# Optimization experiments

Hardware: AMD Instinct MI355X
Metric: run time of the kernel (lower is better)

## Reference

```python
import jax, jax.numpy as jnp
import numpy as np

N_NODES = 60000
N_EDGES = 240000
N_REL = 4
N_GRAPHS = 128
D_IN = 768
D_H = 256
N_LAYERS = 6


def setup_inputs() -> dict:
    key = jax.random.key(0)
    ks = jax.random.split(key, 16)
    x = jax.random.normal(ks[0], (N_NODES, D_IN), dtype=jnp.float32)
    edge_index = jax.random.randint(ks[1], (2, N_EDGES), 0, N_NODES, dtype=jnp.int64)
    edge_attr = jax.random.randint(ks[2], (N_EDGES,), 0, N_REL, dtype=jnp.int64)
    batch = jnp.sort(jax.random.randint(ks[3], (N_NODES,), 0, N_GRAPHS, dtype=jnp.int64))
    s0 = 1.0 / np.sqrt(D_IN)
    s1 = 1.0 / np.sqrt(D_H)
    w0 = jax.random.normal(ks[4], (N_REL, D_IN, D_H), dtype=jnp.float32) * s0
    root0 = jax.random.normal(ks[5], (D_IN, D_H), dtype=jnp.float32) * s0
    b0 = jnp.zeros((D_H,), jnp.float32)
    w_rest = jax.random.normal(ks[6], (N_LAYERS - 1, N_REL, D_H, D_H), dtype=jnp.float32) * s1
    root_rest = jax.random.normal(ks[7], (N_LAYERS - 1, D_H, D_H), dtype=jnp.float32) * s1
    b_rest = jnp.zeros((N_LAYERS - 1, D_H), jnp.float32)
    fc1_w = jax.random.normal(ks[8], (2 * D_H, 128), dtype=jnp.float32) * (1.0 / np.sqrt(2 * D_H))
    fc1_b = jnp.zeros((128,), jnp.float32)
    fc2_w = jax.random.normal(ks[9], (128, 1), dtype=jnp.float32) * (1.0 / np.sqrt(128))
    fc2_b = jnp.zeros((1,), jnp.float32)
    return {"x": x, "edge_index": edge_index, "edge_attr": edge_attr, "batch": batch,
            "w0": w0, "root0": root0, "b0": b0,
            "w_rest": w_rest, "root_rest": root_rest, "b_rest": b_rest,
            "fc1_w": fc1_w, "fc1_b": fc1_b, "fc2_w": fc2_w, "fc2_b": fc2_b}


def _rgcn(h, src, dst, rel, W, root, b):
    # PyG RGCNConv with aggr='mean': per-relation mean over incoming edges,
    # transformed by per-relation weight, plus root transform and bias.
    n = h.shape[0]
    seg = rel * n + dst                                   # combined (relation, target) segment id
    msgs = h[src]                                         # [E, d_in] gather
    agg = jax.ops.segment_sum(msgs, seg, num_segments=N_REL * n)
    agg = agg.reshape(N_REL, n, -1)                       # [R, N, d_in]
    cnt = jax.ops.segment_sum(jnp.ones_like(rel, jnp.float32), seg, num_segments=N_REL * n)
    cnt = cnt.reshape(N_REL, n, 1)
    mean = agg / jnp.maximum(cnt, 1.0)                    # mean aggregation; 0 for isolated nodes
    return jnp.einsum('rnd,rdo->no', mean, W) + h @ root + b


def reference(x, edge_index, edge_attr, batch, w0, root0, b0,
              w_rest, root_rest, b_rest, fc1_w, fc1_b, fc2_w, fc2_b):
    src, dst = edge_index[0], edge_index[1]
    h = jax.nn.relu(_rgcn(x, src, dst, edge_attr, w0, root0, b0))
    for i in range(N_LAYERS - 1):
        h = jax.nn.relu(_rgcn(h, src, dst, edge_attr, w_rest[i], root_rest[i], b_rest[i]))
    # global mean / max pooling over graphs
    sums = jax.ops.segment_sum(h, batch, num_segments=N_GRAPHS)
    cnt = jax.ops.segment_sum(jnp.ones((h.shape[0],), jnp.float32), batch, num_segments=N_GRAPHS)[:, None]
    h_mean = sums / jnp.maximum(cnt, 1.0)
    h_max = jax.ops.segment_max(h, batch, num_segments=N_GRAPHS)
    h_max = jnp.where(cnt > 0, h_max, 0.0)
    g = jnp.concatenate([h_mean, h_max], axis=1)          # [G, 512]
    out = jax.nn.relu(g @ fc1_w + fc1_b)                  # dropout is identity at inference
    out = out @ fc2_w + fc2_b
    return jax.nn.sigmoid(out.squeeze(-1))                # [G]
```

## Files before the change

kernel.cpp:

```cpp
#include <hip/hip_runtime.h>
#include <hip/hip_bf16.h>

#define N_NODES  60000
#define N_EDGES  240000
#define N_REL    4
#define N_GRAPHS 128
#define D_IN     768
#define D_H      256
#define N_LAYERS 6
#define M_PAD    60032
#define N_TOT    1280
#define BM_L     64
#define LDM      264

static inline int cdiv(int a, int b) { return (a + b - 1) / b; }

typedef __attribute__((ext_vector_type(8))) short short8;
typedef __attribute__((ext_vector_type(4))) float f32x4;

__device__ __forceinline__ float bf2f(unsigned short u) {
    union { unsigned int i; float f; } c; c.i = ((unsigned int)u) << 16; return c.f;
}
__device__ __forceinline__ float bflo(unsigned int u) {
    union { unsigned int i; float f; } c; c.i = u << 16; return c.f;
}
__device__ __forceinline__ float bfhi(unsigned int u) {
    union { unsigned int i; float f; } c; c.i = u & 0xffff0000u; return c.f;
}
__device__ __forceinline__ unsigned short f2bf(float f) {
    union { float f; unsigned int i; } c; c.f = f;
    unsigned int i = c.i;
    unsigned int r = (i + 0x7FFFu + ((i >> 16) & 1u)) >> 16;
    return (unsigned short)r;
}

__device__ __forceinline__ void gload16(const void* g, void* l) {
    __builtin_amdgcn_global_load_lds((const __attribute__((address_space(1))) void*)g,
                                     (__attribute__((address_space(3))) void*)l, 16, 0, 0);
}

__device__ __forceinline__ void accum32(float4* am, uint4 v0, uint4 v1, uint4 v2, uint4 v3) {
    am[0].x += bflo(v0.x); am[0].y += bfhi(v0.x);
    am[0].z += bflo(v0.y); am[0].w += bfhi(v0.y);
    am[1].x += bflo(v0.z); am[1].y += bfhi(v0.z);
    am[1].z += bflo(v0.w); am[1].w += bfhi(v0.w);
    am[2].x += bflo(v1.x); am[2].y += bfhi(v1.x);
    am[2].z += bflo(v1.y); am[2].w += bfhi(v1.y);
    am[3].x += bflo(v1.z); am[3].y += bfhi(v1.z);
    am[3].z += bflo(v1.w); am[3].w += bfhi(v1.w);
    am[4].x += bflo(v2.x); am[4].y += bfhi(v2.x);
    am[4].z += bflo(v2.y); am[4].w += bfhi(v2.y);
    am[5].x += bflo(v2.z); am[5].y += bfhi(v2.z);
    am[5].z += bflo(v2.w); am[5].w += bfhi(v2.w);
    am[6].x += bflo(v3.x); am[6].y += bfhi(v3.x);
    am[6].z += bflo(v3.y); am[6].w += bfhi(v3.y);
    am[7].x += bflo(v3.z); am[7].y += bfhi(v3.z);
    am[7].z += bflo(v3.w); am[7].w += bfhi(v3.w);
}

__global__ __launch_bounds__(512) void gemm_l0(
    const unsigned short* __restrict__ A,
    const unsigned short* __restrict__ Bt,
    const float* __restrict__ bias,
    unsigned short* __restrict__ out_root,
    unsigned short* __restrict__ out_msg,
    int K)
{
    __shared__ unsigned short As[128 * 32];
    __shared__ unsigned short Bs[256 * 32];

    const int tid  = threadIdx.x;
    const int wave = tid >> 6, lane = tid & 63;

    int b = blockIdx.x;
    int bm, bn;
    if (b < 2320) { int grp = b / 40, rem = b % 40; bm = (grp * 8 + (rem & 7)) * 128; bn = (rem >> 3) * 256; }
    else          { int rem = b - 2320; bm = (464 + rem % 5) * 128; bn = (rem / 5) * 256; }

    const int wm = (wave & 1) * 64, wn = (wave >> 1) * 64;

    const int lr = lane >> 2;
    const int kg = ((lane & 3) ^ ((lr ^ (lr >> 2)) & 3)) * 8;
    const unsigned short* gsrc[3];
    unsigned short* ldst[3];
    #pragma unroll
    for (int j = 0; j < 3; ++j) {
        int g = wave * 3 + j;
        if (g < 8) {
            gsrc[j] = A + (size_t)(bm + g * 16 + lr) * K + kg;
            ldst[j] = As + g * 16 * 32;
        } else {
            gsrc[j] = Bt + (size_t)(bn + (g - 8) * 16 + lr) * K + kg;
            ldst[j] = Bs + (g - 8) * 16 * 32;
        }
    }

    f32x4 acc[4][4] = {};
    const int fr = lane & 15;
    const int qsw = (((lane >> 4) ^ fr ^ (fr >> 2)) & 3) * 8;

    for (int k0 = 0; k0 < K; k0 += 32) {
        gload16(gsrc[0] + k0, ldst[0]);
        gload16(gsrc[1] + k0, ldst[1]);
        gload16(gsrc[2] + k0, ldst[2]);
        __syncthreads();

        short8 a[4], bb[4];
        #pragma unroll
        for (int t = 0; t < 4; ++t) {
            a[t]  = *(const short8*)&As[(wm + t * 16 + fr) * 32 + qsw];
            bb[t] = *(const short8*)&Bs[(wn + t * 16 + fr) * 32 + qsw];
        }
        #pragma unroll
        for (int mt = 0; mt < 4; ++mt)
            #pragma unroll
            for (int nt = 0; nt < 4; ++nt)
                acc[mt][nt] = __builtin_amdgcn_mfma_f32_16x16x32_bf16(
                    a[mt], bb[nt], acc[mt][nt], 0, 0, 0);
        __syncthreads();
    }

    const bool is_root = (bn == 0);
    #pragma unroll
    for (int mt = 0; mt < 4; ++mt) {
        #pragma unroll
        for (int nt = 0; nt < 4; ++nt) {
            int col = bn + wn + nt * 16 + fr;
            float bv = bias[col];
            #pragma unroll
            for (int r = 0; r < 4; ++r) {
                int row = bm + wm + mt * 16 + ((lane >> 4) << 2) + r;
                float v = acc[mt][nt][r] + bv;
                if (is_root) out_root[(size_t)row * 256 + col] = f2bf(v);
                else         out_msg[(size_t)row * 1024 + (col - 256)] = f2bf(v);
            }
        }
    }
}

__global__ __launch_bounds__(512) void rgcn_layer(
    const unsigned short* __restrict__ h,
    const unsigned short* __restrict__ Wl,
    const float* __restrict__ bias,
    const int* __restrict__ rp4,
    const int* __restrict__ e_srcs,
    const float* __restrict__ inv4,
    unsigned short* __restrict__ h_out)
{
    __shared__ unsigned short mt[BM_L * LDM];
    __shared__ unsigned short Bs[256 * 32];

    const int tid  = threadIdx.x;
    const int wave = tid >> 6, lane = tid & 63;
    const int bm = blockIdx.x * BM_L;

    const int node  = bm + lane;
    const int cq    = wave * 32;
    const bool valid = node < N_NODES;

    const int lr = lane >> 2;
    const int kg = ((lane & 3) ^ ((lr ^ (lr >> 2)) & 3)) * 8;

    const int fr  = lane & 15;
    const int q8  = (lane >> 4) * 8;
    const int qsw = (((lane >> 4) ^ fr ^ (fr >> 2)) & 3) * 8;
    const int wcol = wave * 32;

    float4 iv = valid ? *(const float4*)&inv4[(size_t)node * 4]
                      : make_float4(1.f, 1.f, 1.f, 1.f);

    f32x4 acc[4][2] = {};

    for (int r = 0; r < 5; ++r) {
        float4 am[8];
        #pragma unroll
        for (int j = 0; j < 8; ++j) am[j] = make_float4(0.f, 0.f, 0.f, 0.f);

        if (r < 4) {
            if (valid) {
                int lo = rp4[(size_t)node * 4 + r];
                int hi = rp4[(size_t)node * 4 + r + 1];
                int e = lo;
                for (; e + 1 < hi; e += 2) {
                    const uint4* p0 = (const uint4*)(h + (size_t)e_srcs[e] * 256 + cq);
                    const uint4* p1 = (const uint4*)(h + (size_t)e_srcs[e + 1] * 256 + cq);
                    uint4 v0 = p0[0], v1 = p0[1], v2 = p0[2], v3 = p0[3];
                    uint4 u0 = p1[0], u1 = p1[1], u2 = p1[2], u3 = p1[3];
                    accum32(am, v0, v1, v2, v3);
                    accum32(am, u0, u1, u2, u3);
                }
                if (e < hi) {
                    const uint4* p0 = (const uint4*)(h + (size_t)e_srcs[e] * 256 + cq);
                    accum32(am, p0[0], p0[1], p0[2], p0[3]);
                }
            }
        } else {
            const uint4* p0 = (const uint4*)(h + (size_t)node * 256 + cq);
            accum32(am, p0[0], p0[1], p0[2], p0[3]);
        }
        float sc = (r == 0) ? iv.x : (r == 1) ? iv.y : (r == 2) ? iv.z
                 : (r == 3) ? iv.w : 1.f;

        __syncthreads();
        {
            unsigned short* dst = &mt[lane * LDM + cq];
            #pragma unroll
            for (int j = 0; j < 8; ++j) {
                ushort4 o;
                o.x = f2bf(am[j].x * sc); o.y = f2bf(am[j].y * sc);
                o.z = f2bf(am[j].z * sc); o.w = f2bf(am[j].w * sc);
                *(ushort4*)(dst + j * 4) = o;
            }
        }

        const int rOff = r << 8;
        #pragma unroll 1
        for (int kk = 0; kk < 8; ++kk) {
            if (kk > 0) __syncthreads();
            {
                int g0 = wave * 2;
                gload16(Wl + (size_t)(g0 * 16 + lr) * N_TOT + rOff + kg + kk * 32,
                        Bs + g0 * 512);
                gload16(Wl + (size_t)((g0 + 1) * 16 + lr) * N_TOT + rOff + kg + kk * 32,
                        Bs + (g0 + 1) * 512);
            }
            __syncthreads();

            short8 a4[4], b0, b1;
            #pragma unroll
            for (int i = 0; i < 4; ++i)
                a4[i] = *(const short8*)&mt[(i * 16 + fr) * LDM + kk * 32 + q8];
            b0 = *(const short8*)&Bs[(wcol + fr) * 32 + qsw];
            b1 = *(const short8*)&Bs[(wcol + 16 + fr) * 32 + qsw];
            #pragma unroll
            for (int i = 0; i < 4; ++i) {
                acc[i][0] = __builtin_amdgcn_mfma_f32_16x16x32_bf16(a4[i], b0, acc[i][0], 0, 0, 0);
                acc[i][1] = __builtin_amdgcn_mfma_f32_16x16x32_bf16(a4[i], b1, acc[i][1], 0, 0, 0);
            }
        }
        __syncthreads();
    }

    #pragma unroll
    for (int i = 0; i < 4; ++i) {
        #pragma unroll
        for (int nt = 0; nt < 2; ++nt) {
            int col = wcol + nt * 16 + fr;
            float bv = bias[col];
            #pragma unroll
            for (int rg = 0; rg < 4; ++rg) {
                int row = bm + i * 16 + ((lane >> 4) << 2) + rg;
                float v = fmaxf(acc[i][nt][rg] + bv, 0.f);
                h_out[(size_t)row * 256 + col] = f2bf(v);
            }
        }
    }
}

__global__ void convert_x(const float* __restrict__ x, unsigned short* __restrict__ xb) {
    size_t i = ((size_t)blockIdx.x * 256 + threadIdx.x) * 4;
    if (i >= (size_t)M_PAD * D_IN) return;
    ushort4 o;
    if (i < (size_t)N_NODES * D_IN) {
        float4 v = *(const float4*)&x[i];
        o.x = f2bf(v.x); o.y = f2bf(v.y); o.z = f2bf(v.z); o.w = f2bf(v.w);
    } else {
        o.x = o.y = o.z = o.w = 0;
    }
    *(ushort4*)&xb[i] = o;
}

__global__ __launch_bounds__(256) void pack_w0_t(
    const float* __restrict__ root0, const float* __restrict__ w0,
    unsigned short* __restrict__ Wt0)
{
    __shared__ float t[32][33];
    int b = blockIdx.x;
    int i  = b / 192;
    int rem = b % 192;
    int kb = (rem / 8) * 32;
    int nb = (rem % 8) * 32;
    const float* S = (i == 0) ? root0 : w0 + (size_t)(i - 1) * D_IN * 256;
    int tx = threadIdx.x & 31, ty = threadIdx.x >> 5;
    #pragma unroll
    for (int j = 0; j < 4; ++j)
        t[ty + j * 8][tx] = S[(size_t)(kb + ty + j * 8) * 256 + nb + tx];
    __syncthreads();
    #pragma unroll
    for (int j = 0; j < 4; ++j)
        Wt0[(size_t)(i * 256 + nb + ty + j * 8) * D_IN + kb + tx] = f2bf(t[tx][ty + j * 8]);
}

__global__ __launch_bounds__(256) void pack_wr_t(
    const float* __restrict__ root_rest, const float* __restrict__ w_rest,
    unsigned short* __restrict__ WtR)
{
    __shared__ float t[32][33];
    int b = blockIdx.x;
    int m = b / 64;
    int rem = b % 64;
    int kb = (rem / 8) * 32;
    int nb = (rem % 8) * 32;
    int l = m / 5, j = m % 5;
    const float* S = (j < 4) ? w_rest + (size_t)(l * 4 + j) * 256 * 256
                             : root_rest + (size_t)l * 256 * 256;
    int tx = threadIdx.x & 31, ty = threadIdx.x >> 5;
    #pragma unroll
    for (int jj = 0; jj < 4; ++jj)
        t[ty + jj * 8][tx] = S[(size_t)(kb + ty + jj * 8) * 256 + nb + tx];
    __syncthreads();
    #pragma unroll
    for (int jj = 0; jj < 4; ++jj)
        WtR[(size_t)(l * 256 + nb + ty + jj * 8) * N_TOT + j * 256 + kb + tx] =
            f2bf(t[tx][ty + jj * 8]);
}

__global__ void build_bias(const float* __restrict__ b0, float* __restrict__ eb) {
    int i = blockIdx.x * 256 + threadIdx.x;
    if (i < N_TOT) eb[i] = (i < 256) ? b0[i] : 0.f;
}

__global__ void deg4_count(const int* __restrict__ dst, const int* __restrict__ rel,
                           int* __restrict__ deg4, int E) {
    int e = blockIdx.x * 256 + threadIdx.x;
    if (e < E) atomicAdd(&deg4[dst[e] * 4 + rel[e]], 1);
}

__global__ void invert4(const int* __restrict__ deg4, float* __restrict__ inv4, int n) {
    int i = blockIdx.x * 256 + threadIdx.x;
    if (i < n) inv4[i] = 1.0f / (float)max(deg4[i], 1);
}

__global__ __launch_bounds__(256) void block_sum(const int* __restrict__ deg,
                                                 int* __restrict__ bsum, int n) {
    __shared__ int s[256];
    int i = blockIdx.x * 256 + threadIdx.x;
    s[threadIdx.x] = (i < n) ? deg[i] : 0;
    __syncthreads();
    for (int o = 128; o > 0; o >>= 1) {
        if (threadIdx.x < o) s[threadIdx.x] += s[threadIdx.x + o];
        __syncthreads();
    }
    if (threadIdx.x == 0) bsum[blockIdx.x] = s[0];
}

__global__ __launch_bounds__(1024) void scan_bsum(const int* __restrict__ bsum,
                                                  int* __restrict__ boff, int nb) {
    __shared__ int s[1024];
    int t = threadIdx.x;
    int v0 = (t < nb) ? bsum[t] : 0;
    s[t] = v0;
    __syncthreads();
    for (int o = 1; o < 1024; o <<= 1) {
        int v = (t >= o) ? s[t - o] : 0;
        __syncthreads();
        s[t] += v;
        __syncthreads();
    }
    if (t < nb) boff[t] = s[t] - v0;
}

__global__ __launch_bounds__(256) void block_scan_write(
    const int* __restrict__ deg, const int* __restrict__ boff,
    int* __restrict__ row_ptr, int* __restrict__ cursor, int n, int total) {
    __shared__ int s[256];
    int t = threadIdx.x;
    int i = blockIdx.x * 256 + t;
    int v = (i < n) ? deg[i] : 0;
    s[t] = v;
    __syncthreads();
    for (int o = 1; o < 256; o <<= 1) {
        int u = (t >= o) ? s[t - o] : 0;
        __syncthreads();
        s[t] += u;
        __syncthreads();
    }
    int excl = s[t] - v + boff[blockIdx.x];
    if (i < n) { row_ptr[i] = excl; cursor[i] = excl; }
    if (blockIdx.x == 0 && t == 0) row_ptr[n] = total;
}

__global__ void place_edges4(const int* __restrict__ dst, const int* __restrict__ src,
                             const int* __restrict__ rel, int* __restrict__ cursor,
                             int* __restrict__ e_srcs, int E) {
    int e = blockIdx.x * 256 + threadIdx.x;
    if (e < E) {
        int p = atomicAdd(&cursor[dst[e] * 4 + rel[e]], 1);
        e_srcs[p] = src[e];
    }
}

__global__ __launch_bounds__(256) void aggregate0(
    const unsigned short* __restrict__ rootb,
    const unsigned short* __restrict__ msg,
    const int* __restrict__ rp4, const int* __restrict__ e_srcs,
    const float* __restrict__ inv4,
    unsigned short* __restrict__ h_out)
{
    int node = blockIdx.x * 4 + (threadIdx.x >> 6);
    if (node >= N_NODES) return;
    int lane = threadIdx.x & 63;
    float4 iv = *(const float4*)&inv4[(size_t)node * 4];

    ushort4 rt = *(const ushort4*)&rootb[(size_t)node * 256 + lane * 4];
    float4 acc = make_float4(bf2f(rt.x), bf2f(rt.y), bf2f(rt.z), bf2f(rt.w));

    #pragma unroll
    for (int r = 0; r < 4; ++r) {
        int lo = rp4[(size_t)node * 4 + r], hi = rp4[(size_t)node * 4 + r + 1];
        float f = (r == 0) ? iv.x : (r == 1) ? iv.y : (r == 2) ? iv.z : iv.w;
        float4 s4 = make_float4(0, 0, 0, 0);
        for (int e = lo; e < hi; ++e) {
            int s = e_srcs[e];
            ushort4 m = *(const ushort4*)&msg[(size_t)s * 1024 + (r << 8) + lane * 4];
            s4.x += bf2f(m.x); s4.y += bf2f(m.y);
            s4.z += bf2f(m.z); s4.w += bf2f(m.w);
        }
        acc.x += s4.x * f; acc.y += s4.y * f;
        acc.z += s4.z * f; acc.w += s4.w * f;
    }
    ushort4 o;
    o.x = f2bf(fmaxf(acc.x, 0.f));
    o.y = f2bf(fmaxf(acc.y, 0.f));
    o.z = f2bf(fmaxf(acc.z, 0.f));
    o.w = f2bf(fmaxf(acc.w, 0.f));
    *(ushort4*)&h_out[(size_t)node * 256 + lane * 4] = o;
}

__global__ __launch_bounds__(256) void pool_kernel(
    const unsigned short* __restrict__ h, const int* __restrict__ batch,
    float* __restrict__ g_feat)
{
    int g = blockIdx.x;
    int t = threadIdx.x;
    __shared__ int s_lo, s_hi;
    if (t == 0) {
        int lo = 0, hi = N_NODES;
        while (lo < hi) { int m = (lo + hi) >> 1; if (batch[m] < g) lo = m + 1; else hi = m; }
        s_lo = lo;
        int lo2 = lo, hi2 = N_NODES;
        while (lo2 < hi2) { int m = (lo2 + hi2) >> 1; if (batch[m] < g + 1) lo2 = m + 1; else hi2 = m; }
        s_hi = lo2;
    }
    __syncthreads();
    int lo = s_lo, hi = s_hi;
    float sum = 0.f, mx = 0.f;
    for (int n = lo; n < hi; ++n) {
        float v = bf2f(h[(size_t)n * 256 + t]);
        sum += v;
        mx = fmaxf(mx, v);
    }
    float cnt = (float)(hi - lo);
    g_feat[g * 512 + t]       = sum / fmaxf(cnt, 1.0f);
    g_feat[g * 512 + 256 + t] = (cnt > 0.f) ? mx : 0.f;
}

__global__ __launch_bounds__(128) void mlp_head(
    const float* __restrict__ g_feat,
    const float* __restrict__ fc1_w, const float* __restrict__ fc1_b,
    const float* __restrict__ fc2_w, const float* __restrict__ fc2_b,
    float* __restrict__ out)
{
    __shared__ float gf[512];
    __shared__ float partial[2];
    int g = blockIdx.x, t = threadIdx.x;
    for (int i = t; i < 512; i += 128) gf[i] = g_feat[g * 512 + i];
    __syncthreads();
    float acc = fc1_b[t];
    for (int i = 0; i < 512; ++i) acc += gf[i] * fc1_w[i * 128 + t];
    float h1 = fmaxf(acc, 0.f);
    float v = h1 * fc2_w[t];
    #pragma unroll
    for (int off = 32; off > 0; off >>= 1) v += __shfl_down(v, off);
    if ((t & 63) == 0) partial[t >> 6] = v;
    __syncthreads();
    if (t == 0) {
        float s = partial[0] + partial[1] + fc2_b[0];
        out[g] = 1.0f / (1.0f + expf(-s));
    }
}

extern "C" void kernel_launch(void* const* d_in, const int* in_sizes, int n_in,
                              void* d_out, int out_size, void* d_ws, size_t ws_size,
                              hipStream_t stream) {
    const float* x          = (const float*)d_in[0];
    const int*   edge_index = (const int*)d_in[1];
    const int*   edge_attr  = (const int*)d_in[2];
    const int*   batch      = (const int*)d_in[3];
    const float* w0         = (const float*)d_in[4];
    const float* root0      = (const float*)d_in[5];
    const float* b0         = (const float*)d_in[6];
    const float* w_rest     = (const float*)d_in[7];
    const float* root_rest  = (const float*)d_in[8];
    const float* b_rest     = (const float*)d_in[9];
    const float* fc1_w      = (const float*)d_in[10];
    const float* fc1_b      = (const float*)d_in[11];
    const float* fc2_w      = (const float*)d_in[12];
    const float* fc2_b      = (const float*)d_in[13];
    float* out = (float*)d_out;

    const int* e_src = edge_index;
    const int* e_dst = edge_index + N_EDGES;

    char* p = (char*)d_ws;
    auto alloc = [&](size_t bytes) { char* q = p; p += (bytes + 255) & ~(size_t)255; return q; };
    unsigned short* x_bf   = (unsigned short*)alloc((size_t)M_PAD * D_IN * 2);
    unsigned short* msgbuf = (unsigned short*)alloc((size_t)M_PAD * 1024 * 2);
    unsigned short* hA     = (unsigned short*)alloc((size_t)M_PAD * 256 * 2);
    unsigned short* hB     = (unsigned short*)alloc((size_t)M_PAD * 256 * 2);
    unsigned short* Wt0    = (unsigned short*)alloc((size_t)N_TOT * D_IN * 2);
    unsigned short* WtR    = (unsigned short*)alloc((size_t)5 * 256 * N_TOT * 2);
    float*          ebias  = (float*)alloc(N_TOT * 4);
    float*          inv4   = (float*)alloc((size_t)N_NODES * 4 * 4);
    float*          g_feat = (float*)alloc((size_t)N_GRAPHS * 512 * 4);
    int*            deg4   = (int*)alloc((size_t)N_NODES * 4 * 4);
    int*            rp4    = (int*)alloc(((size_t)N_NODES * 4 + 1) * 4);
    int*            cursor4= (int*)alloc((size_t)N_NODES * 4 * 4);
    int*            bsum   = (int*)alloc(1024 * 4);
    int*            boff   = (int*)alloc(1024 * 4);
    int*            e_srcs = (int*)alloc((size_t)N_EDGES * 4);

    const int n4 = N_NODES * 4;
    const int nscan4 = cdiv(n4, 256);

    hipMemsetAsync(deg4, 0, (size_t)n4 * 4, stream);
    convert_x<<<cdiv(M_PAD * D_IN / 4, 256), 256, 0, stream>>>(x, x_bf);
    pack_w0_t<<<960, 256, 0, stream>>>(root0, w0, Wt0);
    pack_wr_t<<<1600, 256, 0, stream>>>(root_rest, w_rest, WtR);
    build_bias<<<cdiv(N_TOT, 256), 256, 0, stream>>>(b0, ebias);
    deg4_count<<<cdiv(N_EDGES, 256), 256, 0, stream>>>(e_dst, edge_attr, deg4, N_EDGES);
    invert4<<<cdiv(n4, 256), 256, 0, stream>>>(deg4, inv4, n4);
    block_sum<<<nscan4, 256, 0, stream>>>(deg4, bsum, n4);
    scan_bsum<<<1, 1024, 0, stream>>>(bsum, boff, nscan4);
    block_scan_write<<<nscan4, 256, 0, stream>>>(deg4, boff, rp4, cursor4, n4, N_EDGES);
    place_edges4<<<cdiv(N_EDGES, 256), 256, 0, stream>>>(e_dst, e_src, edge_attr,
                                                         cursor4, e_srcs, N_EDGES);

    gemm_l0<<<2345, 512, 0, stream>>>(x_bf, Wt0, ebias, hB, msgbuf, D_IN);
    aggregate0<<<cdiv(N_NODES, 4), 256, 0, stream>>>(hB, msgbuf, rp4, e_srcs, inv4, hA);

    unsigned short* cur = hA;
    unsigned short* nxt = hB;
    for (int L = 1; L < N_LAYERS; ++L) {
        rgcn_layer<<<M_PAD / BM_L, 512, 0, stream>>>(
            cur, WtR + (size_t)(L - 1) * 256 * N_TOT, b_rest + (size_t)(L - 1) * 256,
            rp4, e_srcs, inv4, nxt);
        unsigned short* t = cur; cur = nxt; nxt = t;
    }

    pool_kernel<<<N_GRAPHS, 256, 0, stream>>>(cur, batch, g_feat);
    mlp_head<<<N_GRAPHS, 128, 0, stream>>>(g_feat, fc1_w, fc1_b, fc2_w, fc2_b, out);
}
```

Before: 1.468 ms.

## Split fused RGCN layer into separate aggregation and tiled GEMM kernels

```diff
diff --git a/kernel.cpp b/kernel.cpp
--- a/kernel.cpp
+++ b/kernel.cpp
@@ -10,8 +10,6 @@
 #define N_LAYERS 6
 #define M_PAD    60032
 #define N_TOT    1280
-#define BM_L     64
-#define LDM      264
 
 static inline int cdiv(int a, int b) { return (a + b - 1) / b; }
 
@@ -58,6 +56,25 @@
     am[7].z += bflo(v3.w); am[7].w += bfhi(v3.w);
 }
 
+__device__ __forceinline__ void accum32s(float4* am, uint4 v0, uint4 v1, uint4 v2, uint4 v3, float sc) {
+    am[0].x += bflo(v0.x) * sc; am[0].y += bfhi(v0.x) * sc;
+    am[0].z += bflo(v0.y) * sc; am[0].w += bfhi(v0.y) * sc;
+    am[1].x += bflo(v0.z) * sc; am[1].y += bfhi(v0.z) * sc;
+    am[1].z += bflo(v0.w) * sc; am[1].w += bfhi(v0.w) * sc;
+    am[2].x += bflo(v1.x) * sc; am[2].y += bfhi(v1.x) * sc;
+    am[2].z += bflo(v1.y) * sc; am[2].w += bfhi(v1.y) * sc;
+    am[3].x += bflo(v1.z) * sc; am[3].y += bfhi(v1.z) * sc;
+    am[3].z += bflo(v1.w) * sc; am[3].w += bfhi(v1.w) * sc;
+    am[4].x += bflo(v2.x) * sc; am[4].y += bfhi(v2.x) * sc;
+    am[4].z += bflo(v2.y) * sc; am[4].w += bfhi(v2.y) * sc;
+    am[5].x += bflo(v2.z) * sc; am[5].y += bfhi(v2.z) * sc;
+    am[5].z += bflo(v2.w) * sc; am[5].w += bfhi(v2.w) * sc;
+    am[6].x += bflo(v3.x) * sc; am[6].y += bfhi(v3.x) * sc;
+    am[6].z += bflo(v3.y) * sc; am[6].w += bfhi(v3.y) * sc;
+    am[7].x += bflo(v3.z) * sc; am[7].y += bfhi(v3.z) * sc;
+    am[7].z += bflo(v3.w) * sc; am[7].w += bfhi(v3.w) * sc;
+}
+
 __global__ __launch_bounds__(512) void gemm_l0(
     const unsigned short* __restrict__ A,
     const unsigned short* __restrict__ Bt,
@@ -138,122 +155,210 @@
     }
 }
 
-__global__ __launch_bounds__(512) void rgcn_layer(
+__global__ __launch_bounds__(256) void gemm_mid(
+    const unsigned short* __restrict__ means,
+    const unsigned short* __restrict__ hprev,
+    const unsigned short* __restrict__ Bt,
+    const float* __restrict__ bias,
+    unsigned short* __restrict__ h_out)
+{
+    __shared__ unsigned short As[128 * 32];
+    __shared__ unsigned short Bs[128 * 32];
+
+    const int tid  = threadIdx.x;
+    const int wave = tid >> 6, lane = tid & 63;
+    const int b  = blockIdx.x;
+    const int bm = (b >> 1) * 128;
+    const int bn = (b & 1) * 128;
+    const int wm = (wave & 1) * 64, wn = (wave >> 1) * 64;
+
+    const int lr = lane >> 2;
+    const int kg = ((lane & 3) ^ ((lr ^ (lr >> 2)) & 3)) * 8;
+
+    const unsigned short* srcM[4];
+    const unsigned short* srcH[4];
+    const unsigned short* srcB[4];
+    unsigned short* ldst[4];
+    #pragma unroll
+    for (int j = 0; j < 4; ++j) {
+        int g = wave * 4 + j;
+        if (g < 8) {
+            int row = bm + g * 16 + lr;
+            srcM[j] = means + (size_t)row * 1024 + kg;
+            srcH[j] = hprev + (size_t)row * 256 + kg;
+            srcB[j] = nullptr;
+            ldst[j] = As + g * 512;
+        } else {
+            int row = bn + (g - 8) * 16 + lr;
+            srcB[j] = Bt + (size_t)row * N_TOT + kg;
+            srcM[j] = srcH[j] = nullptr;
+            ldst[j] = Bs + (g - 8) * 512;
+        }
+    }
+
+    f32x4 acc[4][4] = {};
+    const int fr = lane & 15;
+    const int qsw = (((lane >> 4) ^ fr ^ (fr >> 2)) & 3) * 8;
+
+    for (int k0 = 0; k0 < 1024; k0 += 32) {
+        if (wave < 2) {
+            #pragma unroll
+            for (int j = 0; j < 4; ++j) gload16(srcM[j] + k0, ldst[j]);
+        } else {
+            #pragma unroll
+            for (int j = 0; j < 4; ++j) gload16(srcB[j] + k0, ldst[j]);
+        }
+        __syncthreads();
+        short8 a[4], bb[4];
+        #pragma unroll
+        for (int t = 0; t < 4; ++t) {
+            a[t]  = *(const short8*)&As[(wm + t * 16 + fr) * 32 + qsw];
+            bb[t] = *(const short8*)&Bs[(wn + t * 16 + fr) * 32 + qsw];
+        }
+        #pragma unroll
+        for (int mt = 0; mt < 4; ++mt)
+            #pragma unroll
+            for (int nt = 0; nt < 4; ++nt)
+                acc[mt][nt] = __builtin_amdgcn_mfma_f32_16x16x32_bf16(
+                    a[mt], bb[nt], acc[mt][nt], 0, 0, 0);
+        __syncthreads();
+    }
+    for (int k0 = 0; k0 < 256; k0 += 32) {
+        if (wave < 2) {
+            #pragma unroll
+            for (int j = 0; j < 4; ++j) gload16(srcH[j] + k0, ldst[j]);
+        } else {
+            #pragma unroll
+            for (int j = 0; j < 4; ++j) gload16(srcB[j] + 1024 + k0, ldst[j]);
+        }
+        __syncthreads();
+        short8 a[4], bb[4];
+        #pragma unroll
+        for (int t = 0; t < 4; ++t) {
+            a[t]  = *(const short8*)&As[(wm + t * 16 + fr) * 32 + qsw];
+            bb[t] = *(const short8*)&Bs[(wn + t * 16 + fr) * 32 + qsw];
+        }
+        #pragma unroll
+        for (int mt = 0; mt < 4; ++mt)
+            #pragma unroll
+            for (int nt = 0; nt < 4; ++nt)
+                acc[mt][nt] = __builtin_amdgcn_mfma_f32_16x16x32_bf16(
+                    a[mt], bb[nt], acc[mt][nt], 0, 0, 0);
+        __syncthreads();
+    }
+
+    #pragma unroll
+    for (int mt = 0; mt < 4; ++mt) {
+        #pragma unroll
+        for (int nt = 0; nt < 4; ++nt) {
+            int col = bn + wn + nt * 16 + fr;
+            float bv = bias[col];
+            #pragma unroll
+            for (int rg = 0; rg < 4; ++rg) {
+                int row = bm + wm + mt * 16 + ((lane >> 4) << 2) + rg;
+                float v = fmaxf(acc[mt][nt][rg] + bv, 0.f);
+                h_out[(size_t)row * 256 + col] = f2bf(v);
+            }
+        }
+    }
+}
+
+__global__ __launch_bounds__(512) void agg_means(
     const unsigned short* __restrict__ h,
-    const unsigned short* __restrict__ Wl,
-    const float* __restrict__ bias,
-    const int* __restrict__ rp4,
-    const int* __restrict__ e_srcs,
+    const int* __restrict__ rp4, const int* __restrict__ e_sr,
+    const float* __restrict__ inv4,
+    unsigned short* __restrict__ means)
+{
+    const int wave = threadIdx.x >> 6, lane = threadIdx.x & 63;
+    const int node = blockIdx.x * 64 + lane;
+    const int cq = wave * 32;
+    if (node >= N_NODES) return;
+    float4 iv = *(const float4*)&inv4[(size_t)node * 4];
+
+    #pragma unroll
+    for (int r = 0; r < 4; ++r) {
+        float4 am[8];
+        #pragma unroll
+        for (int j = 0; j < 8; ++j) am[j] = make_float4(0.f, 0.f, 0.f, 0.f);
+
+        int lo = rp4[node * 4 + r], hi = rp4[node * 4 + r + 1];
+        int e = lo;
+        for (; e + 1 < hi; e += 2) {
+            int s0 = e_sr[e] & 0xffff, s1 = e_sr[e + 1] & 0xffff;
+            const uint4* p0 = (const uint4*)(h + (size_t)s0 * 256 + cq);
+            const uint4* p1 = (const uint4*)(h + (size_t)s1 * 256 + cq);
+            uint4 a0 = p0[0], a1 = p0[1], a2 = p0[2], a3 = p0[3];
+            uint4 b0 = p1[0], b1 = p1[1], b2 = p1[2], b3 = p1[3];
+            accum32(am, a0, a1, a2, a3);
+            accum32(am, b0, b1, b2, b3);
+        }
+        if (e < hi) {
+            int s0 = e_sr[e] & 0xffff;
+            const uint4* p0 = (const uint4*)(h + (size_t)s0 * 256 + cq);
+            accum32(am, p0[0], p0[1], p0[2], p0[3]);
+        }
+        float sc = (r == 0) ? iv.x : (r == 1) ? iv.y : (r == 2) ? iv.z : iv.w;
+        unsigned short* op = means + (size_t)node * 1024 + (r << 8) + cq;
+        #pragma unroll
+        for (int j = 0; j < 8; ++j) {
+            ushort4 o;
+            o.x = f2bf(am[j].x * sc); o.y = f2bf(am[j].y * sc);
+            o.z = f2bf(am[j].z * sc); o.w = f2bf(am[j].w * sc);
+            *(ushort4*)(op + j * 4) = o;
+        }
+    }
+}
+
+__global__ __launch_bounds__(512) void aggregate0(
+    const unsigned short* __restrict__ rootb,
+    const unsigned short* __restrict__ msg,
+    const int* __restrict__ rp4, const int* __restrict__ e_sr,
     const float* __restrict__ inv4,
     unsigned short* __restrict__ h_out)
 {
-    __shared__ unsigned short mt[BM_L * LDM];
-    __shared__ unsigned short Bs[256 * 32];
-
-    const int tid  = threadIdx.x;
-    const int wave = tid >> 6, lane = tid & 63;
-    const int bm = blockIdx.x * BM_L;
-
-    const int node  = bm + lane;
-    const int cq    = wave * 32;
-    const bool valid = node < N_NODES;
-
-    const int lr = lane >> 2;
-    const int kg = ((lane & 3) ^ ((lr ^ (lr >> 2)) & 3)) * 8;
-
-    const int fr  = lane & 15;
-    const int q8  = (lane >> 4) * 8;
-    const int qsw = (((lane >> 4) ^ fr ^ (fr >> 2)) & 3) * 8;
-    const int wcol = wave * 32;
-
-    float4 iv = valid ? *(const float4*)&inv4[(size_t)node * 4]
-                      : make_float4(1.f, 1.f, 1.f, 1.f);
-
-    f32x4 acc[4][2] = {};
-
-    for (int r = 0; r < 5; ++r) {
-        float4 am[8];
-        #pragma unroll
-        for (int j = 0; j < 8; ++j) am[j] = make_float4(0.f, 0.f, 0.f, 0.f);
-
-        if (r < 4) {
-            if (valid) {
-                int lo = rp4[(size_t)node * 4 + r];
-                int hi = rp4[(size_t)node * 4 + r + 1];
-                int e = lo;
-                for (; e + 1 < hi; e += 2) {
-                    const uint4* p0 = (const uint4*)(h + (size_t)e_srcs[e] * 256 + cq);
-                    const uint4* p1 = (const uint4*)(h + (size_t)e_srcs[e + 1] * 256 + cq);
-                    uint4 v0 = p0[0], v1 = p0[1], v2 = p0[2], v3 = p0[3];
-                    uint4 u0 = p1[0], u1 = p1[1], u2 = p1[2], u3 = p1[3];
-                    accum32(am, v0, v1, v2, v3);
-                    accum32(am, u0, u1, u2, u3);
-                }
-                if (e < hi) {
-                    const uint4* p0 = (const uint4*)(h + (size_t)e_srcs[e] * 256 + cq);
-                    accum32(am, p0[0], p0[1], p0[2], p0[3]);
-                }
-            }
-        } else {
-            const uint4* p0 = (const uint4*)(h + (size_t)node * 256 + cq);
-            accum32(am, p0[0], p0[1], p0[2], p0[3]);
-        }
-        float sc = (r == 0) ? iv.x : (r == 1) ? iv.y : (r == 2) ? iv.z
-                 : (r == 3) ? iv.w : 1.f;
-
-        __syncthreads();
-        {
-            unsigned short* dst = &mt[lane * LDM + cq];
-            #pragma unroll
-            for (int j = 0; j < 8; ++j) {
-                ushort4 o;
-                o.x = f2bf(am[j].x * sc); o.y = f2bf(am[j].y * sc);
-                o.z = f2bf(am[j].z * sc); o.w = f2bf(am[j].w * sc);
-                *(ushort4*)(dst + j * 4) = o;
-            }
-        }
-
-        const int rOff = r << 8;
-        #pragma unroll 1
-        for (int kk = 0; kk < 8; ++kk) {
-            if (kk > 0) __syncthreads();
-            {
-                int g0 = wave * 2;
-                gload16(Wl + (size_t)(g0 * 16 + lr) * N_TOT + rOff + kg + kk * 32,
-                        Bs + g0 * 512);
-                gload16(Wl + (size_t)((g0 + 1) * 16 + lr) * N_TOT + rOff + kg + kk * 32,
-                        Bs + (g0 + 1) * 512);
-            }
-            __syncthreads();
-
-            short8 a4[4], b0, b1;
-            #pragma unroll
-            for (int i = 0; i < 4; ++i)
-                a4[i] = *(const short8*)&mt[(i * 16 + fr) * LDM + kk * 32 + q8];
-            b0 = *(const short8*)&Bs[(wcol + fr) * 32 + qsw];
-            b1 = *(const short8*)&Bs[(wcol + 16 + fr) * 32 + qsw];
-            #pragma unroll
-            for (int i = 0; i < 4; ++i) {
-                acc[i][0] = __builtin_amdgcn_mfma_f32_16x16x32_bf16(a4[i], b0, acc[i][0], 0, 0, 0);
-                acc[i][1] = __builtin_amdgcn_mfma_f32_16x16x32_bf16(a4[i], b1, acc[i][1], 0, 0, 0);
-            }
-        }
-        __syncthreads();
-    }
-
-    #pragma unroll
-    for (int i = 0; i < 4; ++i) {
-        #pragma unroll
-        for (int nt = 0; nt < 2; ++nt) {
-            int col = wcol + nt * 16 + fr;
-            float bv = bias[col];
-            #pragma unroll
-            for (int rg = 0; rg < 4; ++rg) {
-                int row = bm + i * 16 + ((lane >> 4) << 2) + rg;
-                float v = fmaxf(acc[i][nt][rg] + bv, 0.f);
-                h_out[(size_t)row * 256 + col] = f2bf(v);
-            }
-        }
+    const int wave = threadIdx.x >> 6, lane = threadIdx.x & 63;
+    const int node = blockIdx.x * 64 + lane;
+    const int cq = wave * 32;
+    if (node >= N_NODES) return;
+    float4 iv = *(const float4*)&inv4[(size_t)node * 4];
+
+    float4 am[8];
+    #pragma unroll
+    for (int j = 0; j < 8; ++j) am[j] = make_float4(0.f, 0.f, 0.f, 0.f);
+    {
+        const uint4* rp = (const uint4*)(rootb + (size_t)node * 256 + cq);
+        accum32(am, rp[0], rp[1], rp[2], rp[3]);
+    }
+
+    int lo = rp4[node * 4], hi = rp4[node * 4 + 4];
+    int e = lo;
+    for (; e + 1 < hi; e += 2) {
+        int sr0 = e_sr[e], sr1 = e_sr[e + 1];
+        int s0 = sr0 & 0xffff, r0 = sr0 >> 16;
+        int s1 = sr1 & 0xffff, r1 = sr1 >> 16;
+        float c0 = (r0 == 0) ? iv.x : (r0 == 1) ? iv.y : (r0 == 2) ? iv.z : iv.w;
+        float c1 = (r1 == 0) ? iv.x : (r1 == 1) ? iv.y : (r1 == 2) ? iv.z : iv.w;
+        const uint4* p0 = (const uint4*)(msg + (size_t)s0 * 1024 + (r0 << 8) + cq);
+        const uint4* p1 = (const uint4*)(msg + (size_t)s1 * 1024 + (r1 << 8) + cq);
+        uint4 a0 = p0[0], a1 = p0[1], a2 = p0[2], a3 = p0[3];
+        uint4 b0 = p1[0], b1 = p1[1], b2 = p1[2], b3 = p1[3];
+        accum32s(am, a0, a1, a2, a3, c0);
+        accum32s(am, b0, b1, b2, b3, c1);
+    }
+    if (e < hi) {
+        int sr0 = e_sr[e];
+        int s0 = sr0 & 0xffff, r0 = sr0 >> 16;
+        float c0 = (r0 == 0) ? iv.x : (r0 == 1) ? iv.y : (r0 == 2) ? iv.z : iv.w;
+        const uint4* p0 = (const uint4*)(msg + (size_t)s0 * 1024 + (r0 << 8) + cq);
+        accum32s(am, p0[0], p0[1], p0[2], p0[3], c0);
+    }
+    unsigned short* op = h_out + (size_t)node * 256 + cq;
+    #pragma unroll
+    for (int j = 0; j < 8; ++j) {
+        ushort4 o;
+        o.x = f2bf(fmaxf(am[j].x, 0.f)); o.y = f2bf(fmaxf(am[j].y, 0.f));
+        o.z = f2bf(fmaxf(am[j].z, 0.f)); o.w = f2bf(fmaxf(am[j].w, 0.f));
+        *(ushort4*)(op + j * 4) = o;
     }
 }
 
@@ -382,49 +487,13 @@
 
 __global__ void place_edges4(const int* __restrict__ dst, const int* __restrict__ src,
                              const int* __restrict__ rel, int* __restrict__ cursor,
-                             int* __restrict__ e_srcs, int E) {
+                             int* __restrict__ e_sr, int E) {
     int e = blockIdx.x * 256 + threadIdx.x;
     if (e < E) {
-        int p = atomicAdd(&cursor[dst[e] * 4 + rel[e]], 1);
-        e_srcs[p] = src[e];
-    }
-}
-
-__global__ __launch_bounds__(256) void aggregate0(
-    const unsigned short* __restrict__ rootb,
-    const unsigned short* __restrict__ msg,
-    const int* __restrict__ rp4, const int* __restrict__ e_srcs,
-    const float* __restrict__ inv4,
-    unsigned short* __restrict__ h_out)
-{
-    int node = blockIdx.x * 4 + (threadIdx.x >> 6);
-    if (node >= N_NODES) return;
-    int lane = threadIdx.x & 63;
-    float4 iv = *(const float4*)&inv4[(size_t)node * 4];
-
-    ushort4 rt = *(const ushort4*)&rootb[(size_t)node * 256 + lane * 4];
-    float4 acc = make_float4(bf2f(rt.x), bf2f(rt.y), bf2f(rt.z), bf2f(rt.w));
-
-    #pragma unroll
-    for (int r = 0; r < 4; ++r) {
-        int lo = rp4[(size_t)node * 4 + r], hi = rp4[(size_t)node * 4 + r + 1];
-        float f = (r == 0) ? iv.x : (r == 1) ? iv.y : (r == 2) ? iv.z : iv.w;
-        float4 s4 = make_float4(0, 0, 0, 0);
-        for (int e = lo; e < hi; ++e) {
-            int s = e_srcs[e];
-            ushort4 m = *(const ushort4*)&msg[(size_t)s * 1024 + (r << 8) + lane * 4];
-            s4.x += bf2f(m.x); s4.y += bf2f(m.y);
-            s4.z += bf2f(m.z); s4.w += bf2f(m.w);
-        }
-        acc.x += s4.x * f; acc.y += s4.y * f;
-        acc.z += s4.z * f; acc.w += s4.w * f;
-    }
-    ushort4 o;
-    o.x = f2bf(fmaxf(acc.x, 0.f));
-    o.y = f2bf(fmaxf(acc.y, 0.f));
-    o.z = f2bf(fmaxf(acc.z, 0.f));
-    o.w = f2bf(fmaxf(acc.w, 0.f));
-    *(ushort4*)&h_out[(size_t)node * 256 + lane * 4] = o;
+        int d = dst[e], r = rel[e], s = src[e];
+        int pI = atomicAdd(&cursor[d * 4 + r], 1);
+        e_sr[pI] = s | (r << 16);
+    }
 }
 
 __global__ __launch_bounds__(256) void pool_kernel(
@@ -518,10 +587,11 @@
     int*            cursor4= (int*)alloc((size_t)N_NODES * 4 * 4);
     int*            bsum   = (int*)alloc(1024 * 4);
     int*            boff   = (int*)alloc(1024 * 4);
-    int*            e_srcs = (int*)alloc((size_t)N_EDGES * 4);
+    int*            e_sr   = (int*)alloc((size_t)N_EDGES * 4);
 
     const int n4 = N_NODES * 4;
     const int nscan4 = cdiv(n4, 256);
+    const int ngrid = cdiv(N_NODES, 64);
 
     hipMemsetAsync(deg4, 0, (size_t)n4 * 4, stream);
     convert_x<<<cdiv(M_PAD * D_IN / 4, 256), 256, 0, stream>>>(x, x_bf);
@@ -534,17 +604,18 @@
     scan_bsum<<<1, 1024, 0, stream>>>(bsum, boff, nscan4);
     block_scan_write<<<nscan4, 256, 0, stream>>>(deg4, boff, rp4, cursor4, n4, N_EDGES);
     place_edges4<<<cdiv(N_EDGES, 256), 256, 0, stream>>>(e_dst, e_src, edge_attr,
-                                                         cursor4, e_srcs, N_EDGES);
+                                                         cursor4, e_sr, N_EDGES);
 
     gemm_l0<<<2345, 512, 0, stream>>>(x_bf, Wt0, ebias, hB, msgbuf, D_IN);
-    aggregate0<<<cdiv(N_NODES, 4), 256, 0, stream>>>(hB, msgbuf, rp4, e_srcs, inv4, hA);
+    aggregate0<<<ngrid, 512, 0, stream>>>(hB, msgbuf, rp4, e_sr, inv4, hA);
 
     unsigned short* cur = hA;
     unsigned short* nxt = hB;
     for (int L = 1; L < N_LAYERS; ++L) {
-        rgcn_layer<<<M_PAD / BM_L, 512, 0, stream>>>(
-            cur, WtR + (size_t)(L - 1) * 256 * N_TOT, b_rest + (size_t)(L - 1) * 256,
-            rp4, e_srcs, inv4, nxt);
+        agg_means<<<ngrid, 512, 0, stream>>>(cur, rp4, e_sr, inv4, msgbuf);
+        gemm_mid<<<2 * (M_PAD / 128), 256, 0, stream>>>(
+            msgbuf, cur, WtR + (size_t)(L - 1) * 256 * N_TOT,
+            b_rest + (size_t)(L - 1) * 256, nxt);
         unsigned short* t = cur; cur = nxt; nxt = t;
     }
 
```

New measurement: 1.351 ms. 1.09x faster.
